# Optimization experiments

Hardware: AMD Instinct MI355X
Metric: run time of the kernel (lower is better)

Reference implementation:

```python
import jax, jax.numpy as jnp
from jax import lax
import numpy as np

F_IN, H, B, T = 257, 512, 16, 1024
ATTN_LEN = 128


def _lstm(x, w_ih, w_hh, b_ih, b_hh):
    """torch-style LSTM over time axis. x: (B,T,H). gate order i,f,g,o."""
    xg = jnp.einsum('bth,gh->btg', x, w_ih) + b_ih  # (B,T,4H)

    def step(carry, xg_t):
        h, c = carry
        g = xg_t + h @ w_hh.T + b_hh
        i, f, gg, o = jnp.split(g, 4, axis=-1)
        c = jax.nn.sigmoid(f) * c + jax.nn.sigmoid(i) * jnp.tanh(gg)
        h = jax.nn.sigmoid(o) * jnp.tanh(c)
        return (h, c), h

    h0 = jnp.zeros((x.shape[0], w_hh.shape[1]), x.dtype)
    _, hs = lax.scan(step, (h0, h0), jnp.swapaxes(xg, 0, 1))
    return jnp.swapaxes(hs, 0, 1)  # (B,T,H)


def setup_inputs() -> dict:
    key = jax.random.key(0)
    ks = jax.random.split(key, 16)
    sF = 1.0 / np.sqrt(F_IN)
    sH = 1.0 / np.sqrt(H)
    inp = {
        'x': jax.random.normal(ks[0], (B, T, F_IN), jnp.float32),
        'feat_w': jax.random.normal(ks[1], (H, F_IN), jnp.float32) * sF,
        'feat_b': jnp.zeros((H,), jnp.float32),
        'k_w_ih': jax.random.normal(ks[2], (4 * H, H), jnp.float32) * sH,
        'k_w_hh': jax.random.normal(ks[3], (4 * H, H), jnp.float32) * sH,
        'k_b_ih': jnp.zeros((4 * H,), jnp.float32),
        'k_b_hh': jnp.zeros((4 * H,), jnp.float32),
        'q_w_ih': jax.random.normal(ks[4], (4 * H, H), jnp.float32) * sH,
        'q_w_hh': jax.random.normal(ks[5], (4 * H, H), jnp.float32) * sH,
        'q_b_ih': jnp.zeros((4 * H,), jnp.float32),
        'q_b_hh': jnp.zeros((4 * H,), jnp.float32),
        'score_w': jax.random.normal(ks[6], (H, H), jnp.float32) * sH,
        'enh_w': jax.random.normal(ks[7], (H, 2 * H), jnp.float32) * (1.0 / np.sqrt(2 * H)),
        'enh_b': jnp.zeros((H,), jnp.float32),
        'mask_w': jax.random.normal(ks[8], (F_IN, H), jnp.float32) * sH,
        'mask_b': jnp.zeros((F_IN,), jnp.float32),
    }
    return inp


def reference(x, feat_w, feat_b, k_w_ih, k_w_hh, k_b_ih, k_b_hh,
              q_w_ih, q_w_hh, q_b_ih, q_b_hh, score_w,
              enh_w, enh_b, mask_w, mask_b):
    input_x = x
    xf = x @ feat_w.T + feat_b                       # (B,T,H)
    k = _lstm(xf, k_w_ih, k_w_hh, k_b_ih, k_b_hh)    # (B,T,H)
    q = _lstm(xf, q_w_ih, q_w_hh, q_b_ih, q_b_hh)    # stacked_encoder=False -> q_enc(x)

    # causal banded exp-attention, no max-subtraction (faithful to source)
    scores = jnp.einsum('bth,bsh->bts', q @ score_w.T, k)  # (B,T,T)
    t_idx = jnp.arange(T)
    band = (t_idx[None, :] <= t_idx[:, None]) & (t_idx[None, :] >= t_idx[:, None] - ATTN_LEN)
    attn = jnp.where(band[None], jnp.exp(scores), 0.0)
    attn = attn / (jnp.sum(attn, axis=-1, keepdims=True) + 1e-10)
    c = jnp.einsum('bts,bsh->bth', attn, k)          # (B,T,H)

    out = jnp.concatenate([c, q], axis=-1)           # (B,T,2H)
    out = jnp.tanh(out @ enh_w.T + enh_b)
    out = jax.nn.sigmoid(out @ mask_w.T + mask_b)    # (B,T,F)
    return (input_x * out, attn)
```

## Files before the change

kernel.cpp:

```cpp
#include <hip/hip_runtime.h>
#include <hip/hip_bf16.h>
#include <math.h>

#define B_ 16
#define T_ 1024
#define F_ 257
#define H_ 512
#define BT (B_*T_)
#define ALEN 128
#define LSTM_NWG 256

static const size_t OFF_A    = 0;
static const size_t OFF_B    = OFF_A + (size_t)BT*H_;
static const size_t OFF_C    = OFF_B + (size_t)BT*H_;
static const size_t OFF_HB   = OFF_C + (size_t)BT*H_;
static const size_t OFF_SUB  = OFF_HB + 32768;
static const size_t OFF_MST  = OFF_SUB + 16384;
static const size_t WS_NEED  = OFF_MST + 2048;

__device__ __forceinline__ float sigmoidf_(float v) { return 1.0f / (1.0f + expf(-v)); }

template<int ACT>
__global__ __launch_bounds__(256)
void gemm_kernel(const float* __restrict__ A1, const float* __restrict__ A2, int K1,
                 const float* __restrict__ W, const float* __restrict__ bias1,
                 const float* __restrict__ bias2, const float* __restrict__ xmul,
                 float* __restrict__ C, int M, int N, int K)
{
    __shared__ __align__(16) float As[16][68];
    __shared__ __align__(16) float Ws[16][68];
    int tid = threadIdx.x;
    int tx = tid & 15, ty = tid >> 4;
    int m0 = blockIdx.y * 64, n0 = blockIdx.x * 64;
    int lrow = tid >> 2, lk = (tid & 3) * 4;
    float acc[4][4] = {};
    int ntiles = (K + 15) >> 4;
    int ldA2 = K - K1;
    for (int kt = 0; kt < ntiles; ++kt) {
        int k0 = kt << 4;
        #pragma unroll
        for (int j = 0; j < 4; ++j) {
            int k = k0 + lk + j;
            float av = 0.0f, wv = 0.0f;
            if (k < K) {
                int m = m0 + lrow;
                av = (k < K1) ? A1[(size_t)m * K1 + k] : A2[(size_t)m * ldA2 + (k - K1)];
                int n = n0 + lrow;
                if (n < N) wv = W[(size_t)n * K + k];
            }
            As[lk + j][lrow] = av;
            Ws[lk + j][lrow] = wv;
        }
        __syncthreads();
        #pragma unroll
        for (int kk = 0; kk < 16; ++kk) {
            float4 a = *(const float4*)&As[kk][ty * 4];
            float4 w = *(const float4*)&Ws[kk][tx * 4];
            acc[0][0] += a.x * w.x; acc[0][1] += a.x * w.y; acc[0][2] += a.x * w.z; acc[0][3] += a.x * w.w;
            acc[1][0] += a.y * w.x; acc[1][1] += a.y * w.y; acc[1][2] += a.y * w.z; acc[1][3] += a.y * w.w;
            acc[2][0] += a.z * w.x; acc[2][1] += a.z * w.y; acc[2][2] += a.z * w.z; acc[2][3] += a.z * w.w;
            acc[3][0] += a.w * w.x; acc[3][1] += a.w * w.y; acc[3][2] += a.w * w.z; acc[3][3] += a.w * w.w;
        }
        __syncthreads();
    }
    #pragma unroll
    for (int i = 0; i < 4; ++i) {
        int m = m0 + ty * 4 + i;
        #pragma unroll
        for (int j = 0; j < 4; ++j) {
            int n = n0 + tx * 4 + j;
            if (n < N) {
                float v = acc[i][j];
                if (bias1) v += bias1[n];
                if (bias2) v += bias2[n];
                if (ACT == 1) v = tanhf(v);
                if (ACT == 2) v = sigmoidf_(v) * xmul[(size_t)m * N + n];
                if (ACT == 3) {
                    C[((size_t)(m & 1023) << 13) + ((size_t)n << 4) + (m >> 10)] = v;
                } else {
                    C[(size_t)m * N + n] = v;
                }
            }
        }
    }
}

__global__ __launch_bounds__(512, 2)
void lstm_fused(const float* __restrict__ xf_t,
                const float* __restrict__ k_wih, const float* __restrict__ k_whh,
                const float* __restrict__ k_bih, const float* __restrict__ k_bhh,
                const float* __restrict__ q_wih, const float* __restrict__ q_whh,
                const float* __restrict__ q_bih, const float* __restrict__ q_bhh,
                float* __restrict__ k_out, float* __restrict__ q_out,
                float* __restrict__ hbuf, int* __restrict__ sub, int* __restrict__ mst)
{
    const int wg = blockIdx.x, tid = threadIdx.x;
    const int lstm = wg >> 7;
    const int u0 = (wg & 127) * 4;
    const int grp = (wg & 127) >> 4;
    const float* wih = lstm ? q_wih : k_wih;
    const float* whh = lstm ? q_whh : k_whh;
    const float* bih = lstm ? q_bih : k_bih;
    const float* bhh = lstm ? q_bhh : k_bhh;
    float* out = lstm ? q_out : k_out;
    float* hb = hbuf + lstm * 16384;
    int* subc = sub + ((lstm * 8 + grp) << 10);
    int* mstc = mst + (lstm << 10);

    const int wv = tid >> 6, lane = tid & 63;
    const int cg = lane & 3, bg = (lane >> 2) & 3, ks = lane >> 4;

    float4 wreg[4][8];
    {
        const float* Wsrc = (wv < 4) ? wih : whh;
        const int kbase = (wv & 3) * 128 + ks * 32;
        #pragma unroll
        for (int j = 0; j < 4; ++j) {
            const float4* wp = (const float4*)(Wsrc + ((size_t)(j * 512 + u0 + cg) << 9) + kbase);
            #pragma unroll
            for (int i = 0; i < 8; ++i) wreg[j][i] = wp[i];
        }
    }

    __shared__ __align__(16) float vec[16384];
    __shared__ float part[16][16][33];
    __shared__ float gsum[256];

    const int cu = tid & 3, cb = tid >> 2;
    float bI = 0.f, bF = 0.f, bG = 0.f, bO = 0.f, cst = 0.f;
    if (tid < 64) {
        bI = bih[0 * 512 + u0 + cu] + bhh[0 * 512 + u0 + cu];
        bF = bih[1 * 512 + u0 + cu] + bhh[1 * 512 + u0 + cu];
        bG = bih[2 * 512 + u0 + cu] + bhh[2 * 512 + u0 + cu];
        bO = bih[3 * 512 + u0 + cu] + bhh[3 * 512 + u0 + cu];
    }

    float4 xfr0, xfr1, xfr2, xfr3;
    {
        const float4* xs = (const float4*)xf_t;
        xfr0 = xs[0 * 512 + tid]; xfr1 = xs[1 * 512 + tid];
        xfr2 = xs[2 * 512 + tid]; xfr3 = xs[3 * 512 + tid];
    }

    for (int t = 0; t < T_; ++t) {
        const int rb = t & 1;
        {
            float4* vd = (float4*)vec;
            vd[0 * 512 + tid] = xfr0;
            vd[1 * 512 + tid] = xfr1;
            vd[2 * 512 + tid] = xfr2;
            vd[3 * 512 + tid] = xfr3;
            const float4* hp = (const float4*)(hb + rb * 8192);
            const float4* p0 = hp + 0 * 512 + tid;
            const float4* p1 = hp + 1 * 512 + tid;
            const float4* p2 = hp + 2 * 512 + tid;
            const float4* p3 = hp + 3 * 512 + tid;
            float4 h0, h1, h2, h3;
            asm volatile(
                "global_load_dwordx4 %0, %4, off sc0 sc1\n\t"
                "global_load_dwordx4 %1, %5, off sc0 sc1\n\t"
                "global_load_dwordx4 %2, %6, off sc0 sc1\n\t"
                "global_load_dwordx4 %3, %7, off sc0 sc1\n\t"
                "s_waitcnt vmcnt(0)"
                : "=&v"(h0), "=&v"(h1), "=&v"(h2), "=&v"(h3)
                : "v"(p0), "v"(p1), "v"(p2), "v"(p3)
                : "memory");
            vd[2048 + 0 * 512 + tid] = h0;
            vd[2048 + 1 * 512 + tid] = h1;
            vd[2048 + 2 * 512 + tid] = h2;
            vd[2048 + 3 * 512 + tid] = h3;
            if (t + 1 < T_) {
                const float4* xs2 = (const float4*)(xf_t + ((size_t)(t + 1) << 13));
                xfr0 = xs2[0 * 512 + tid]; xfr1 = xs2[1 * 512 + tid];
                xfr2 = xs2[2 * 512 + tid]; xfr3 = xs2[3 * 512 + tid];
            }
        }
        __syncthreads();

        float4 a0 = {0,0,0,0}, a1 = {0,0,0,0}, a2 = {0,0,0,0}, a3 = {0,0,0,0};
        {
            const float4* vb = ((const float4*)vec) + (((size_t)wv * 128 + ks * 32) << 2) + bg;
            #pragma unroll
            for (int i = 0; i < 8; ++i) {
                float4 v0 = vb[(i * 4 + 0) * 4];
                float4 v1 = vb[(i * 4 + 1) * 4];
                float4 v2 = vb[(i * 4 + 2) * 4];
                float4 v3 = vb[(i * 4 + 3) * 4];
                float4 w;
                #define FMA4_(A) \
                    A.x += w.x * v0.x + w.y * v1.x + w.z * v2.x + w.w * v3.x; \
                    A.y += w.x * v0.y + w.y * v1.y + w.z * v2.y + w.w * v3.y; \
                    A.z += w.x * v0.z + w.y * v1.z + w.z * v2.z + w.w * v3.z; \
                    A.w += w.x * v0.w + w.y * v1.w + w.z * v2.w + w.w * v3.w;
                w = wreg[0][i]; FMA4_(a0)
                w = wreg[1][i]; FMA4_(a1)
                w = wreg[2][i]; FMA4_(a2)
                w = wreg[3][i]; FMA4_(a3)
                #undef FMA4_
            }
        }
        {
            const int s = wv * 4 + ks, c0 = cg * 4, bq = bg * 4;
            part[c0 + 0][bq + 0][s] = a0.x; part[c0 + 0][bq + 1][s] = a0.y;
            part[c0 + 0][bq + 2][s] = a0.z; part[c0 + 0][bq + 3][s] = a0.w;
            part[c0 + 1][bq + 0][s] = a1.x; part[c0 + 1][bq + 1][s] = a1.y;
            part[c0 + 1][bq + 2][s] = a1.z; part[c0 + 1][bq + 3][s] = a1.w;
            part[c0 + 2][bq + 0][s] = a2.x; part[c0 + 2][bq + 1][s] = a2.y;
            part[c0 + 2][bq + 2][s] = a2.z; part[c0 + 2][bq + 3][s] = a2.w;
            part[c0 + 3][bq + 0][s] = a3.x; part[c0 + 3][bq + 1][s] = a3.y;
            part[c0 + 3][bq + 2][s] = a3.z; part[c0 + 3][bq + 3][s] = a3.w;
        }
        __syncthreads();

        if (tid < 256) {
            const int c = tid >> 4, b = tid & 15;
            float s = 0.f;
            #pragma unroll
            for (int ss = 0; ss < 32; ++ss) s += part[c][b][ss];
            gsum[c * 16 + b] = s;
        }
        __syncthreads();

        if (tid < 64) {
            float gI = bI + gsum[(cu * 4 + 0) * 16 + cb];
            float gF = bF + gsum[(cu * 4 + 1) * 16 + cb];
            float gG = bG + gsum[(cu * 4 + 2) * 16 + cb];
            float gO = bO + gsum[(cu * 4 + 3) * 16 + cb];
            float ig = sigmoidf_(gI), fg = sigmoidf_(gF), gg = tanhf(gG), og = sigmoidf_(gO);
            cst = fg * cst + ig * gg;
            float h = og * tanhf(cst);
            __hip_atomic_store(&hb[(rb ^ 1) * 8192 + ((u0 + cu) << 4) + cb], h,
                               __ATOMIC_RELAXED, __HIP_MEMORY_SCOPE_SYSTEM);
            out[((size_t)(cb * T_ + t) << 9) + (u0 + cu)] = h;
        }
        asm volatile("s_waitcnt vmcnt(0)" ::: "memory");
        __syncthreads();
        if (tid == 0) {
            int old = __hip_atomic_fetch_add(&subc[t], 1, __ATOMIC_RELAXED, __HIP_MEMORY_SCOPE_AGENT);
            if (old == 15)
                __hip_atomic_fetch_add(&mstc[t], 1, __ATOMIC_RELAXED, __HIP_MEMORY_SCOPE_AGENT);
            while (__hip_atomic_load(&mstc[t], __ATOMIC_RELAXED, __HIP_MEMORY_SCOPE_SYSTEM) < 8)
                __builtin_amdgcn_s_sleep(2);
        }
        __syncthreads();
    }
}

__global__ __launch_bounds__(256)
void attn_scores(const float* __restrict__ qs, const float* __restrict__ kk,
                 float* __restrict__ attn_out)
{
    int t = blockIdx.x, b = blockIdx.y, tid = threadIdx.x;
    int jlo = t - ALEN; if (jlo < 0) jlo = 0;
    int cnt = t - jlo + 1;
    __shared__ __align__(16) float qrow[512];
    __shared__ float sc[132];
    __shared__ float ssum;
    const float* qsr = qs + ((size_t)(b * T_ + t) << 9);
    qrow[tid] = qsr[tid];
    qrow[tid + 256] = qsr[tid + 256];
    __syncthreads();
    if (tid < cnt) {
        const float4* krow = (const float4*)(kk + ((size_t)(b * T_ + jlo + tid) << 9));
        const float4* q4 = (const float4*)qrow;
        float acc = 0.f;
        #pragma unroll 4
        for (int i = 0; i < 128; ++i) {
            float4 kv = krow[i]; float4 qv = q4[i];
            acc += kv.x * qv.x + kv.y * qv.y + kv.z * qv.z + kv.w * qv.w;
        }
        sc[tid] = expf(acc);
    }
    __syncthreads();
    if (tid < 64) {
        float s = 0.f;
        for (int j = tid; j < cnt; j += 64) s += sc[j];
        #pragma unroll
        for (int off = 32; off > 0; off >>= 1) s += __shfl_down(s, off);
        if (tid == 0) ssum = s + 1e-10f;
    }
    __syncthreads();
    float inv = 1.0f / ssum;
    float4* arow = (float4*)(attn_out + ((size_t)(b * T_ + t) << 10));
    int j0 = tid * 4;
    float4 v;
    v.x = (j0 + 0 >= jlo && j0 + 0 <= t) ? sc[j0 + 0 - jlo] * inv : 0.f;
    v.y = (j0 + 1 >= jlo && j0 + 1 <= t) ? sc[j0 + 1 - jlo] * inv : 0.f;
    v.z = (j0 + 2 >= jlo && j0 + 2 <= t) ? sc[j0 + 2 - jlo] * inv : 0.f;
    v.w = (j0 + 3 >= jlo && j0 + 3 <= t) ? sc[j0 + 3 - jlo] * inv : 0.f;
    arow[tid] = v;
}

__global__ __launch_bounds__(256)
void attn_ctx(const float* __restrict__ attn, const float* __restrict__ kk,
              float* __restrict__ c_out)
{
    int t = blockIdx.x, b = blockIdx.y, tid = threadIdx.x;
    int jlo = t - ALEN; if (jlo < 0) jlo = 0;
    int cnt = t - jlo + 1;
    __shared__ float sc[132];
    if (tid < cnt) sc[tid] = attn[((size_t)(b * T_ + t) << 10) + jlo + tid];
    __syncthreads();
    #pragma unroll
    for (int hh = 0; hh < 2; ++hh) {
        int h = tid + hh * 256;
        const float* kcol = kk + ((size_t)(b * T_ + jlo) << 9) + h;
        float acc = 0.f;
        #pragma unroll 4
        for (int jj = 0; jj < cnt; ++jj) acc += sc[jj] * kcol[(size_t)jj << 9];
        c_out[((size_t)(b * T_ + t) << 9) + h] = acc;
    }
}

extern "C" void kernel_launch(void* const* d_in, const int* in_sizes, int n_in,
                              void* d_out_v, int out_size, void* d_ws, size_t ws_size,
                              hipStream_t stream)
{
    const float* x       = (const float*)d_in[0];
    const float* feat_w  = (const float*)d_in[1];
    const float* feat_b  = (const float*)d_in[2];
    const float* k_w_ih  = (const float*)d_in[3];
    const float* k_w_hh  = (const float*)d_in[4];
    const float* k_b_ih  = (const float*)d_in[5];
    const float* k_b_hh  = (const float*)d_in[6];
    const float* q_w_ih  = (const float*)d_in[7];
    const float* q_w_hh  = (const float*)d_in[8];
    const float* q_b_ih  = (const float*)d_in[9];
    const float* q_b_hh  = (const float*)d_in[10];
    const float* score_w = (const float*)d_in[11];
    const float* enh_w   = (const float*)d_in[12];
    const float* enh_b   = (const float*)d_in[13];
    const float* mask_w  = (const float*)d_in[14];
    const float* mask_b  = (const float*)d_in[15];
    float* out = (float*)d_out_v;
    float* ws  = (float*)d_ws;

    if (ws_size < WS_NEED * sizeof(float)) return;

    float* bufA = ws + OFF_A;
    float* bufB = ws + OFF_B;
    float* bufC = ws + OFF_C;
    float* hbuf = ws + OFF_HB;
    int*   sub  = (int*)(ws + OFF_SUB);
    int*   mst  = (int*)(ws + OFF_MST);

    hipMemsetAsync(hbuf, 0, (32768 + 16384 + 2048) * sizeof(float), stream);

    dim3 blk(256);
    gemm_kernel<3><<<dim3(8, 256), blk, 0, stream>>>(x, nullptr, F_, feat_w, feat_b, nullptr, nullptr, bufA, BT, H_, F_);
    lstm_fused<<<dim3(LSTM_NWG), dim3(512), 0, stream>>>(bufA,
        k_w_ih, k_w_hh, k_b_ih, k_b_hh, q_w_ih, q_w_hh, q_b_ih, q_b_hh,
        bufB, bufC, hbuf, sub, mst);
    gemm_kernel<0><<<dim3(8, 256), blk, 0, stream>>>(bufC, nullptr, H_, score_w, nullptr, nullptr, nullptr, bufA, BT, H_, H_);
    attn_scores<<<dim3(T_, B_), blk, 0, stream>>>(bufA, bufB, out + (size_t)BT * F_);
    attn_ctx<<<dim3(T_, B_), blk, 0, stream>>>(out + (size_t)BT * F_, bufB, bufA);
    gemm_kernel<1><<<dim3(8, 256), blk, 0, stream>>>(bufA, bufC, H_, enh_w, enh_b, nullptr, nullptr, bufB, BT, H_, 2 * H_);
    gemm_kernel<2><<<dim3(5, 256), blk, 0, stream>>>(bufB, nullptr, H_, mask_w, mask_b, nullptr, x, out, BT, F_, H_);
}
```

Baseline: 8.044 ms.

## Split LSTM waves so input-projection waves overlap the cross-workgroup barrier

Waves 0-3 now stage only the precomputed xf input and start their input-weight dot products right away. Only waves 4-7, which need h from the previous step, wait on the grid-level arrival counter, through one polling wave and an LDS ready flag. The end-of-step spin and the two block barriers around it are removed, so the input half of each step overlaps the global synchronisation. LDS rows are padded to avoid bank conflicts and the weight registers are written as named scalars. The trade-off is subtler memory ordering, since there is an intra-workgroup flag and a store to LDS before the tid0 atomic with no barrier between them.

```diff
diff --git a/kernel.cpp b/kernel.cpp
--- a/kernel.cpp
+++ b/kernel.cpp
@@ -110,21 +110,28 @@
     const int wv = tid >> 6, lane = tid & 63;
     const int cg = lane & 3, bg = (lane >> 2) & 3, ks = lane >> 4;
 
-    float4 wreg[4][8];
+    float4 w00,w01,w02,w03,w04,w05,w06,w07;
+    float4 w10,w11,w12,w13,w14,w15,w16,w17;
+    float4 w20,w21,w22,w23,w24,w25,w26,w27;
+    float4 w30,w31,w32,w33,w34,w35,w36,w37;
     {
         const float* Wsrc = (wv < 4) ? wih : whh;
-        const int kbase = (wv & 3) * 128 + ks * 32;
-        #pragma unroll
-        for (int j = 0; j < 4; ++j) {
-            const float4* wp = (const float4*)(Wsrc + ((size_t)(j * 512 + u0 + cg) << 9) + kbase);
-            #pragma unroll
-            for (int i = 0; i < 8; ++i) wreg[j][i] = wp[i];
-        }
-    }
-
-    __shared__ __align__(16) float vec[16384];
+        const int kb = (wv & 3) * 128 + ks * 32;
+        const float4* p;
+        p = (const float4*)(Wsrc + ((size_t)(0 * 512 + u0 + cg) << 9) + kb);
+        w00=p[0];w01=p[1];w02=p[2];w03=p[3];w04=p[4];w05=p[5];w06=p[6];w07=p[7];
+        p = (const float4*)(Wsrc + ((size_t)(1 * 512 + u0 + cg) << 9) + kb);
+        w10=p[0];w11=p[1];w12=p[2];w13=p[3];w14=p[4];w15=p[5];w16=p[6];w17=p[7];
+        p = (const float4*)(Wsrc + ((size_t)(2 * 512 + u0 + cg) << 9) + kb);
+        w20=p[0];w21=p[1];w22=p[2];w23=p[3];w24=p[4];w25=p[5];w26=p[6];w27=p[7];
+        p = (const float4*)(Wsrc + ((size_t)(3 * 512 + u0 + cg) << 9) + kb);
+        w30=p[0];w31=p[1];w32=p[2];w33=p[3];w34=p[4];w35=p[5];w36=p[6];w37=p[7];
+    }
+
+    __shared__ __align__(16) float4 vec4[4160];
     __shared__ float part[16][16][33];
     __shared__ float gsum[256];
+    __shared__ int ready;
 
     const int cu = tid & 3, cb = tid >> 2;
     float bI = 0.f, bF = 0.f, bG = 0.f, bO = 0.f, cst = 0.f;
@@ -134,71 +141,98 @@
         bG = bih[2 * 512 + u0 + cu] + bhh[2 * 512 + u0 + cu];
         bO = bih[3 * 512 + u0 + cu] + bhh[3 * 512 + u0 + cu];
     }
-
-    float4 xfr0, xfr1, xfr2, xfr3;
-    {
-        const float4* xs = (const float4*)xf_t;
-        xfr0 = xs[0 * 512 + tid]; xfr1 = xs[1 * 512 + tid];
-        xfr2 = xs[2 * 512 + tid]; xfr3 = xs[3 * 512 + tid];
-    }
+    if (tid == 0) ready = 0;
+
+    float4 xf0{},xf1{},xf2{},xf3{},xf4{},xf5{},xf6{},xf7{};
+    if (wv < 4) {
+        const float4* xs = (const float4*)xf_t + (wv << 9) + lane;
+        xf0=xs[0];  xf1=xs[64];  xf2=xs[128]; xf3=xs[192];
+        xf4=xs[256];xf5=xs[320]; xf6=xs[384]; xf7=xs[448];
+    }
+    __syncthreads();
 
     for (int t = 0; t < T_; ++t) {
         const int rb = t & 1;
-        {
-            float4* vd = (float4*)vec;
-            vd[0 * 512 + tid] = xfr0;
-            vd[1 * 512 + tid] = xfr1;
-            vd[2 * 512 + tid] = xfr2;
-            vd[3 * 512 + tid] = xfr3;
-            const float4* hp = (const float4*)(hb + rb * 8192);
-            const float4* p0 = hp + 0 * 512 + tid;
-            const float4* p1 = hp + 1 * 512 + tid;
-            const float4* p2 = hp + 2 * 512 + tid;
-            const float4* p3 = hp + 3 * 512 + tid;
-            float4 h0, h1, h2, h3;
+        float4 a0{},a1{},a2{},a3{};
+        const float4* vb;
+        if (wv < 4) {
+            const int xb = wv * 520;
+            vec4[xb +   0 + lane] = xf0;
+            vec4[xb +  64 + lane] = xf1;
+            vec4[xb + 130 + lane] = xf2;
+            vec4[xb + 194 + lane] = xf3;
+            vec4[xb + 260 + lane] = xf4;
+            vec4[xb + 324 + lane] = xf5;
+            vec4[xb + 390 + lane] = xf6;
+            vec4[xb + 454 + lane] = xf7;
+            if (t + 1 < T_) {
+                const float4* xs = (const float4*)(xf_t + ((size_t)(t + 1) << 13)) + (wv << 9) + lane;
+                xf0=xs[0];  xf1=xs[64];  xf2=xs[128]; xf3=xs[192];
+                xf4=xs[256];xf5=xs[320]; xf6=xs[384]; xf7=xs[448];
+            }
+            asm volatile("s_waitcnt lgkmcnt(0)" ::: "memory");
+            vb = vec4 + xb + ks * 130 + bg;
+        } else {
+            if (t > 0) {
+                if (wv == 4) {
+                    while (__hip_atomic_load(&mstc[t - 1], __ATOMIC_RELAXED, __HIP_MEMORY_SCOPE_SYSTEM) < 8)
+                        __builtin_amdgcn_s_sleep(2);
+                    if (lane == 0)
+                        __hip_atomic_store(&ready, t, __ATOMIC_RELAXED, __HIP_MEMORY_SCOPE_WORKGROUP);
+                } else {
+                    while (__hip_atomic_load(&ready, __ATOMIC_RELAXED, __HIP_MEMORY_SCOPE_WORKGROUP) < t)
+                        __builtin_amdgcn_s_sleep(1);
+                }
+            }
+            const float4* hp  = (const float4*)(hb + rb * 8192) + ((wv - 4) << 9) + lane;
+            const float4* hp2 = hp + 256;
+            float4 h0,h1,h2,h3,h4,h5,h6,h7;
             asm volatile(
-                "global_load_dwordx4 %0, %4, off sc0 sc1\n\t"
-                "global_load_dwordx4 %1, %5, off sc0 sc1\n\t"
-                "global_load_dwordx4 %2, %6, off sc0 sc1\n\t"
-                "global_load_dwordx4 %3, %7, off sc0 sc1\n\t"
+                "global_load_dwordx4 %0, %8, off sc0 sc1\n\t"
+                "global_load_dwordx4 %1, %8, off offset:1024 sc0 sc1\n\t"
+                "global_load_dwordx4 %2, %8, off offset:2048 sc0 sc1\n\t"
+                "global_load_dwordx4 %3, %8, off offset:3072 sc0 sc1\n\t"
+                "global_load_dwordx4 %4, %9, off sc0 sc1\n\t"
+                "global_load_dwordx4 %5, %9, off offset:1024 sc0 sc1\n\t"
+                "global_load_dwordx4 %6, %9, off offset:2048 sc0 sc1\n\t"
+                "global_load_dwordx4 %7, %9, off offset:3072 sc0 sc1\n\t"
                 "s_waitcnt vmcnt(0)"
-                : "=&v"(h0), "=&v"(h1), "=&v"(h2), "=&v"(h3)
-                : "v"(p0), "v"(p1), "v"(p2), "v"(p3)
+                : "=&v"(h0),"=&v"(h1),"=&v"(h2),"=&v"(h3),
+                  "=&v"(h4),"=&v"(h5),"=&v"(h6),"=&v"(h7)
+                : "v"(hp), "v"(hp2)
                 : "memory");
-            vd[2048 + 0 * 512 + tid] = h0;
-            vd[2048 + 1 * 512 + tid] = h1;
-            vd[2048 + 2 * 512 + tid] = h2;
-            vd[2048 + 3 * 512 + tid] = h3;
-            if (t + 1 < T_) {
-                const float4* xs2 = (const float4*)(xf_t + ((size_t)(t + 1) << 13));
-                xfr0 = xs2[0 * 512 + tid]; xfr1 = xs2[1 * 512 + tid];
-                xfr2 = xs2[2 * 512 + tid]; xfr3 = xs2[3 * 512 + tid];
-            }
-        }
-        __syncthreads();
-
-        float4 a0 = {0,0,0,0}, a1 = {0,0,0,0}, a2 = {0,0,0,0}, a3 = {0,0,0,0};
-        {
-            const float4* vb = ((const float4*)vec) + (((size_t)wv * 128 + ks * 32) << 2) + bg;
-            #pragma unroll
-            for (int i = 0; i < 8; ++i) {
-                float4 v0 = vb[(i * 4 + 0) * 4];
-                float4 v1 = vb[(i * 4 + 1) * 4];
-                float4 v2 = vb[(i * 4 + 2) * 4];
-                float4 v3 = vb[(i * 4 + 3) * 4];
-                float4 w;
-                #define FMA4_(A) \
-                    A.x += w.x * v0.x + w.y * v1.x + w.z * v2.x + w.w * v3.x; \
-                    A.y += w.x * v0.y + w.y * v1.y + w.z * v2.y + w.w * v3.y; \
-                    A.z += w.x * v0.z + w.y * v1.z + w.z * v2.z + w.w * v3.z; \
-                    A.w += w.x * v0.w + w.y * v1.w + w.z * v2.w + w.w * v3.w;
-                w = wreg[0][i]; FMA4_(a0)
-                w = wreg[1][i]; FMA4_(a1)
-                w = wreg[2][i]; FMA4_(a2)
-                w = wreg[3][i]; FMA4_(a3)
-                #undef FMA4_
-            }
-        }
+            const int hbv = 2080 + (wv - 4) * 520;
+            vec4[hbv +   0 + lane] = h0;
+            vec4[hbv +  64 + lane] = h1;
+            vec4[hbv + 130 + lane] = h2;
+            vec4[hbv + 194 + lane] = h3;
+            vec4[hbv + 260 + lane] = h4;
+            vec4[hbv + 324 + lane] = h5;
+            vec4[hbv + 390 + lane] = h6;
+            vec4[hbv + 454 + lane] = h7;
+            asm volatile("s_waitcnt lgkmcnt(0)" ::: "memory");
+            vb = vec4 + hbv + ks * 130 + bg;
+        }
+
+        #define FMA4_(A, W) \
+            A.x += W.x*v0.x + W.y*v1.x + W.z*v2.x + W.w*v3.x; \
+            A.y += W.x*v0.y + W.y*v1.y + W.z*v2.y + W.w*v3.y; \
+            A.z += W.x*v0.z + W.y*v1.z + W.z*v2.z + W.w*v3.z; \
+            A.w += W.x*v0.w + W.y*v1.w + W.z*v2.w + W.w*v3.w;
+        #define FSTEP(i, WA, WB, WC, WD) { \
+            float4 v0 = vb[(i)*16], v1 = vb[(i)*16+4], v2 = vb[(i)*16+8], v3 = vb[(i)*16+12]; \
+            FMA4_(a0, WA) FMA4_(a1, WB) FMA4_(a2, WC) FMA4_(a3, WD) }
+        FSTEP(0, w00,w10,w20,w30)
+        FSTEP(1, w01,w11,w21,w31)
+        FSTEP(2, w02,w12,w22,w32)
+        FSTEP(3, w03,w13,w23,w33)
+        FSTEP(4, w04,w14,w24,w34)
+        FSTEP(5, w05,w15,w25,w35)
+        FSTEP(6, w06,w16,w26,w36)
+        FSTEP(7, w07,w17,w27,w37)
+        #undef FSTEP
+        #undef FMA4_
+
         {
             const int s = wv * 4 + ks, c0 = cg * 4, bq = bg * 4;
             part[c0 + 0][bq + 0][s] = a0.x; part[c0 + 0][bq + 1][s] = a0.y;
@@ -214,10 +248,10 @@
 
         if (tid < 256) {
             const int c = tid >> 4, b = tid & 15;
-            float s = 0.f;
+            float s2 = 0.f;
             #pragma unroll
-            for (int ss = 0; ss < 32; ++ss) s += part[c][b][ss];
-            gsum[c * 16 + b] = s;
+            for (int ss = 0; ss < 32; ++ss) s2 += part[c][b][ss];
+            gsum[c * 16 + b] = s2;
         }
         __syncthreads();
 
@@ -229,20 +263,16 @@
             float ig = sigmoidf_(gI), fg = sigmoidf_(gF), gg = tanhf(gG), og = sigmoidf_(gO);
             cst = fg * cst + ig * gg;
             float h = og * tanhf(cst);
-            __hip_atomic_store(&hb[(rb ^ 1) * 8192 + ((u0 + cu) << 4) + cb], h,
+            __hip_atomic_store(&hb[((rb ^ 1) << 13) + ((u0 + cu) << 4) + cb], h,
                                __ATOMIC_RELAXED, __HIP_MEMORY_SCOPE_SYSTEM);
             out[((size_t)(cb * T_ + t) << 9) + (u0 + cu)] = h;
-        }
-        asm volatile("s_waitcnt vmcnt(0)" ::: "memory");
-        __syncthreads();
+            asm volatile("s_waitcnt vmcnt(0)" ::: "memory");
+        }
         if (tid == 0) {
             int old = __hip_atomic_fetch_add(&subc[t], 1, __ATOMIC_RELAXED, __HIP_MEMORY_SCOPE_AGENT);
             if (old == 15)
                 __hip_atomic_fetch_add(&mstc[t], 1, __ATOMIC_RELAXED, __HIP_MEMORY_SCOPE_AGENT);
-            while (__hip_atomic_load(&mstc[t], __ATOMIC_RELAXED, __HIP_MEMORY_SCOPE_SYSTEM) < 8)
-                __builtin_amdgcn_s_sleep(2);
-        }
-        __syncthreads();
+        }
     }
 }
 
```

New measurement: 7.968 ms. About the same (-0.9%).
